# Optimization experiments

Hardware: AMD Instinct MI355X
Metric: run time of the kernel (lower is better)

## Reference

```python
import math
import jax, jax.numpy as jnp
import numpy as np

V, D, DEPTH, S, B = 32000, 1024, 4, 512, 2
N, K = 16, 4            # ssm state_dim, d_conv
R = math.ceil(D / 16)   # dt_rank ('auto') = 64
MLP = 4 * D


def _ln(x, s, b):
    m = jnp.mean(x, -1, keepdims=True)
    v = jnp.mean((x - m) ** 2, -1, keepdims=True)
    return (x - m) * jax.lax.rsqrt(v + 1e-5) * s + b


def _dwconv(x, w):
    # x: [B,S,D], w: [D,1,K]; causal depthwise conv (torch pads K-1 both sides then slices [:S])
    xt = jnp.transpose(x, (0, 2, 1))  # [B,D,S]
    y = jax.lax.conv_general_dilated(
        xt, w, window_strides=(1,), padding=[(K - 1, 0)],
        feature_group_count=D, dimension_numbers=('NCH', 'OIH', 'NCH'))
    return jnp.transpose(y, (0, 2, 1))


def _ssm(x, zw, pw, cw, dw, db, al, dpar, ow):
    z = x @ zw.T                     # [B,S,D]
    p = x @ pw.T                     # [B,S,R+2N]
    dt_un, Bp, Cp = p[..., :R], p[..., R:R + N], p[..., R + N:]
    dt = jax.nn.softplus(dt_un @ dw.T + db)          # [B,S,D]
    u = jax.nn.silu(_dwconv(x, cw))                  # [B,S,D]
    A = -jnp.exp(al)                                 # [D,N]
    At = jnp.exp(dt[..., None] * A)                  # [B,S,D,N]
    Bt = jnp.where(jnp.abs(A) < 1e-8, dt[..., None], (At - 1.0) / (A + 1e-10))
    inp = jnp.einsum('bsdn,bsn,bsd->bsdn', Bt, Bp, u)

    def step(h, xs):
        At_t, inp_t, C_t = xs
        h = At_t * h + inp_t
        return h, jnp.einsum('bn,bdn->bd', C_t, h)

    h0 = jnp.zeros((x.shape[0], D, N), x.dtype)
    _, ys = jax.lax.scan(step, h0, (jnp.moveaxis(At, 1, 0), jnp.moveaxis(inp, 1, 0), jnp.moveaxis(Cp, 1, 0)))
    y = jnp.moveaxis(ys, 0, 1)                       # [B,S,D]
    y = (y + u * dpar) * jax.nn.silu(z)
    return y @ ow.T


def _forward(input_ids, timesteps, tok_emb, time_w1, time_b1, time_w2, time_b2,
             norm1_s, norm1_b, xW, zW, pW, convW, dtW, dtb, A_log, Dp, outW,
             norm2_s, norm2_b, mlpW1, mlpb1, mlpW2, mlpb2, normo_s, normo_b, headW, headb):
    half = D // 2
    inv = jnp.exp(-(math.log(10000.0) / half) * jnp.arange(half, dtype=jnp.float32))
    args = timesteps.astype(jnp.float32)[:, None] * inv
    temb = jnp.concatenate([jnp.sin(args), jnp.cos(args)], axis=-1)        # [B,D]
    temb = jax.nn.silu(temb @ time_w1.T + time_b1) @ time_w2.T + time_b2
    x = tok_emb[input_ids] + temb[:, None, :]                              # [B,S,D]

    def block(x, prm):
        n1s, n1b, zw, pw, cw, dw, db, al, dpar, ow, n2s, n2b, w1, b1, w2, b2 = prm
        x = x + _ssm(_ln(x, n1s, n1b), zw, pw, cw, dw, db, al, dpar, ow)
        xn = _ln(x, n2s, n2b)
        x = x + (jax.nn.gelu(xn @ w1.T + b1, approximate=False) @ w2.T + b2)
        return x, None

    stacked = (norm1_s, norm1_b, zW, pW, convW, dtW, dtb, A_log, Dp, outW,
               norm2_s, norm2_b, mlpW1, mlpb1, mlpW2, mlpb2)
    x, _ = jax.lax.scan(block, x, stacked)
    x = _ln(x, normo_s, normo_b)
    return x @ headW.T + headb  # [B,S,V]


def setup_inputs():
    key = jax.random.key(0)
    ks = jax.random.split(key, 24)
    rn = lambda k, sh, sc=0.02: jax.random.normal(k, sh, jnp.float32) * sc
    dt_std = R ** (-0.5) * 0.1
    inp = {
        'input_ids': jax.random.randint(ks[0], (B, S), 0, V + 1),
        'timesteps': jax.random.randint(ks[1], (B,), 0, 100),
        'tok_emb': rn(ks[2], (V + 1, D)),
        'time_w1': rn(ks[3], (4 * D, D)), 'time_b1': jnp.zeros((4 * D,), jnp.float32),
        'time_w2': rn(ks[4], (D, 4 * D)), 'time_b2': jnp.zeros((D,), jnp.float32),
        'norm1_s': jnp.ones((DEPTH, D), jnp.float32), 'norm1_b': jnp.zeros((DEPTH, D), jnp.float32),
        'xW': rn(ks[5], (DEPTH, D, D)),   # in_proj_x (dead in forward, grad=0)
        'zW': rn(ks[6], (DEPTH, D, D)),
        'pW': rn(ks[7], (DEPTH, R + 2 * N, D)),
        'convW': rn(ks[8], (DEPTH, D, 1, K), 0.1),
        'dtW': jax.random.uniform(ks[9], (DEPTH, D, R), jnp.float32, -dt_std, dt_std),
        'dtb': jnp.full((DEPTH, D), math.log(math.expm1(0.001)), jnp.float32),
        'A_log': jnp.tile(jnp.log(jnp.arange(1, N + 1, dtype=jnp.float32))[None, None, :], (DEPTH, D, 1)),
        'Dp': jnp.ones((DEPTH, D), jnp.float32),
        'outW': rn(ks[10], (DEPTH, D, D)),
        'norm2_s': jnp.ones((DEPTH, D), jnp.float32), 'norm2_b': jnp.zeros((DEPTH, D), jnp.float32),
        'mlpW1': rn(ks[11], (DEPTH, MLP, D)), 'mlpb1': jnp.zeros((DEPTH, MLP), jnp.float32),
        'mlpW2': rn(ks[12], (DEPTH, D, MLP)), 'mlpb2': jnp.zeros((DEPTH, D), jnp.float32),
        'normo_s': jnp.ones((D,), jnp.float32), 'normo_b': jnp.zeros((D,), jnp.float32),
        'headW': rn(ks[13], (V, D)), 'headb': jnp.zeros((V,), jnp.float32),
    }
    return inp


def reference(input_ids, timesteps, tok_emb, time_w1, time_b1, time_w2, time_b2,
              norm1_s, norm1_b, xW, zW, pW, convW, dtW, dtb, A_log, Dp, outW,
              norm2_s, norm2_b, mlpW1, mlpb1, mlpW2, mlpb2, normo_s, normo_b, headW, headb):
    return _forward(input_ids, timesteps, tok_emb, time_w1, time_b1, time_w2, time_b2,
                    norm1_s, norm1_b, xW, zW, pW, convW, dtW, dtb, A_log, Dp, outW,
                    norm2_s, norm2_b, mlpW1, mlpb1, mlpW2, mlpb2, normo_s, normo_b, headW, headb)
```

## Files before the change

kernel.cpp:

```cpp
#include <hip/hip_runtime.h>
#include <math.h>


#define DEV __device__ __forceinline__
typedef unsigned int u32;
typedef unsigned short ushort;
typedef __bf16 bf16x8 __attribute__((ext_vector_type(8)));
typedef float f32x4 __attribute__((ext_vector_type(4)));
typedef ushort us8 __attribute__((ext_vector_type(8)));

DEV float silu_f(float x){ return x / (1.f + expf(-x)); }
DEV float gelu_f(float x){ return 0.5f * x * (1.f + erff(x * 0.70710678118654752f)); }
DEV float softplus_f(float x){ return (x > 20.f) ? x : log1pf(expf(x)); }
DEV ushort f2b(float f){
  u32 u = __builtin_bit_cast(u32, f);
  return (ushort)((u + 0x7fffu + ((u >> 16) & 1u)) >> 16);
}
DEV float b2f(ushort u){ return __builtin_bit_cast(float, (u32)u << 16); }

DEV void gl_lds16(const ushort* g, ushort* l){
  __builtin_amdgcn_global_load_lds(
      (const __attribute__((address_space(1))) u32*)g,
      (__attribute__((address_space(3))) u32*)l, 16, 0, 0);
}

DEV void cvt_layer_unit(u32 j, const float* zWl, const float* pWl, const float* oWl,
                        const float* m1Wl, const float* m2Wl, ushort* wl)
{
  const float* src; u32 sj, dj;
  if (j < 294912u){
    dj = j;
    u32 row = j >> 8;
    if (row < 1024u){ src = zWl; sj = j; }
    else {
      u32 pr = row - 1024u;
      if (pr >= 96u){ ushort4 z4 = {0,0,0,0}; ((ushort4*)wl)[dj] = z4; return; }
      src = pWl; sj = pr*256u + (j & 255u);
    }
  } else if (j < 557056u){ u32 k = j - 294912u;  dj = j; src = oWl;  sj = k; }
  else if (j < 1605632u){ u32 k = j - 557056u;  dj = j; src = m1Wl; sj = k; }
  else                  { u32 k = j - 1605632u; dj = j; src = m2Wl; sj = k; }
  float4 v = ((const float4*)src)[sj];
  ushort4 o4; o4.x=f2b(v.x); o4.y=f2b(v.y); o4.z=f2b(v.z); o4.w=f2b(v.w);
  ((ushort4*)wl)[dj] = o4;
}

__global__ __launch_bounds__(256) void k_cvtmega(
    const float* __restrict__ zW, const float* __restrict__ pW,
    const float* __restrict__ oW, const float* __restrict__ m1W,
    const float* __restrict__ m2W, const float* __restrict__ hW,
    ushort* __restrict__ wall, ushort* __restrict__ whb)
{
  u32 i = blockIdx.x*256u + threadIdx.x;
  if (i >= 18808832u) return;
  if (i >= 10616832u){
    u32 j = i - 10616832u;
    float4 v = ((const float4*)hW)[j];
    ushort4 o4; o4.x=f2b(v.x); o4.y=f2b(v.y); o4.z=f2b(v.z); o4.w=f2b(v.w);
    ((ushort4*)whb)[j] = o4;
    return;
  }
  u32 l = i / 2654208u;
  u32 j = i - l*2654208u;
  cvt_layer_unit(j, zW + (size_t)l*1048576u, pW + (size_t)l*98304u,
                 oW + (size_t)l*1048576u, m1W + (size_t)l*4194304u,
                 m2W + (size_t)l*4194304u, wall + (size_t)l*10616832u);
}

__global__ __launch_bounds__(256) void k_cvtall(
    const float* __restrict__ zWl, const float* __restrict__ pWl,
    const float* __restrict__ oWl, const float* __restrict__ m1Wl,
    const float* __restrict__ m2Wl, ushort* __restrict__ wl)
{
  u32 j = blockIdx.x*256u + threadIdx.x;
  if (j >= 2654208u) return;
  cvt_layer_unit(j, zWl, pWl, oWl, m1Wl, m2Wl, wl);
}

__global__ __launch_bounds__(256) void k_cvt(const float* __restrict__ in, ushort* __restrict__ out, int n4){
  int i = blockIdx.x*256 + threadIdx.x;
  if (i >= n4) return;
  float4 v = ((const float4*)in)[i];
  ushort4 o; o.x=f2b(v.x); o.y=f2b(v.y); o.z=f2b(v.z); o.w=f2b(v.w);
  ((ushort4*)out)[i] = o;
}

__global__ __launch_bounds__(256) void k_temb1m(const int* __restrict__ ts, const float* __restrict__ w1,
                                                const float* __restrict__ b1, float* __restrict__ t1){
  __shared__ float sXT[1024];
  int bid = blockIdx.x;
  int tid = threadIdx.x;
  int b = (bid*4) >> 12;
  float tv = (float)ts[b];
  #pragma unroll
  for (int k=0;k<4;k++){
    int j = tid + k*256;
    int i = j & 511;
    float arg = tv * expf(-(9.210340371976184f/512.f) * (float)i);
    sXT[j] = (j < 512) ? sinf(arg) : cosf(arg);
  }
  __syncthreads();
  int o = bid*4 + (tid >> 6);
  int lane = tid & 63;
  int j = o & 4095;
  const float4* xr = (const float4*)sXT;
  const float4* wr = (const float4*)(w1 + (size_t)j*1024);
  float acc = 0.f;
  #pragma unroll
  for (int i=0;i<4;i++){
    float4 x4 = xr[i*64 + lane], w4 = wr[i*64 + lane];
    acc += x4.x*w4.x + x4.y*w4.y + x4.z*w4.z + x4.w*w4.w;
  }
  #pragma unroll
  for (int off=32; off; off>>=1) acc += __shfl_down(acc, off);
  if (lane==0) t1[o] = silu_f(acc + b1[j]);
}

__global__ __launch_bounds__(256) void k_temb2(const float* __restrict__ t1, const float* __restrict__ w2,
                                               const float* __restrict__ b2, float* __restrict__ t2){
  int o = blockIdx.x*4 + (threadIdx.x >> 6);
  int lane = threadIdx.x & 63;
  int b = o >> 10, j = o & 1023;
  const float4* xr = (const float4*)(t1 + b*4096);
  const float4* wr = (const float4*)(w2 + (size_t)j*4096);
  float acc = 0.f;
  #pragma unroll
  for (int i=0;i<16;i++){
    float4 x4 = xr[i*64 + lane], w4 = wr[i*64 + lane];
    acc += x4.x*w4.x + x4.y*w4.y + x4.z*w4.z + x4.w*w4.w;
  }
  #pragma unroll
  for (int off=32; off; off>>=1) acc += __shfl_down(acc, off);
  if (lane==0) t2[o] = acc + b2[j];
}

DEV void ln_body(float4 v, const float* sc, const float* bi, int row, int t,
                 float* o, ushort* obf)
{
  float sum = v.x+v.y+v.z+v.w;
  float sq  = v.x*v.x+v.y*v.y+v.z*v.z+v.w*v.w;
  for (int o_=32;o_;o_>>=1){ sum += __shfl_down(sum,o_); sq += __shfl_down(sq,o_); }
  __shared__ float ps[8];
  int lane = t & 63, wid = t >> 6;
  if (lane==0){ ps[wid]=sum; ps[4+wid]=sq; }
  __syncthreads();
  float tot = ps[0]+ps[1]+ps[2]+ps[3];
  float tsq = ps[4]+ps[5]+ps[6]+ps[7];
  float m = tot * (1.f/1024.f);
  float var = tsq*(1.f/1024.f) - m*m;
  float r = rsqrtf(var + 1e-5f);
  float4 s4 = ((const float4*)sc)[t];
  float4 b4 = ((const float4*)bi)[t];
  float4 o4;
  o4.x = (v.x-m)*r*s4.x + b4.x;
  o4.y = (v.y-m)*r*s4.y + b4.y;
  o4.z = (v.z-m)*r*s4.z + b4.z;
  o4.w = (v.w-m)*r*s4.w + b4.w;
  ((float4*)(o + (size_t)row*1024))[t] = o4;
  ushort4 ob; ob.x=f2b(o4.x); ob.y=f2b(o4.y); ob.z=f2b(o4.z); ob.w=f2b(o4.w);
  ((ushort4*)(obf + (size_t)row*1024))[t] = ob;
}

__global__ __launch_bounds__(256) void k_ln(const float* __restrict__ x, const float* __restrict__ sc,
                                            const float* __restrict__ bi, float* __restrict__ o,
                                            ushort* __restrict__ obf){
  int row = blockIdx.x, t = threadIdx.x;
  float4 v = ((const float4*)(x + (size_t)row*1024))[t];
  ln_body(v, sc, bi, row, t, o, obf);
}

__global__ __launch_bounds__(256) void k_embln(const int* __restrict__ ids, const float* __restrict__ tok,
                                               const float* __restrict__ t2, const float* __restrict__ sc,
                                               const float* __restrict__ bi, float* __restrict__ xout,
                                               float* __restrict__ o, ushort* __restrict__ obf){
  int row = blockIdx.x, t = threadIdx.x;
  int id = ids[row];
  float4 v = ((const float4*)(tok + (size_t)id*1024))[t];
  float4 e = ((const float4*)(t2 + ((row >> 9) << 10)))[t];
  v.x += e.x; v.y += e.y; v.z += e.z; v.w += e.w;
  ((float4*)(xout + (size_t)row*1024))[t] = v;
  ln_body(v, sc, bi, row, t, o, obf);
}

__global__ __launch_bounds__(512) void k_scanf(
    const ushort* __restrict__ pb64, const float* __restrict__ dtW, const float* __restrict__ dtb,
    const float* __restrict__ xn, const float* __restrict__ p, const float* __restrict__ alog,
    const float* __restrict__ z, const float* __restrict__ Dp,
    const float* __restrict__ cw, ushort* __restrict__ y2b)
{
  const int bid = blockIdx.x;
  const int logical = (bid & 7)*256 + (bid >> 3);
  const int d = logical & 1023;
  const int b = logical >> 10;
  const int tid = threadIdx.x;
  const int c = tid >> 4, n = tid & 15;
  const float al = alog[d*16 + n];
  const float A = -expf(al);
  const float invA = 1.f/(A + 1e-10f);
  const bool tiny = fabsf(A) < 1e-8f;
  const float dscale = Dp[d];
  const float cw0 = cw[d*4], cw1 = cw[d*4+1], cw2 = cw[d*4+2], cw3 = cw[d*4+3];
  const size_t base = (size_t)b*512*1024 + d;
  const float* pp = p + (size_t)b*512*96;
  const int s0 = c*16;

  __shared__ float sXN[520];
  __shared__ float sDT[512], sZ[512];
  __shared__ float sA[512], sB[512], sH[512];
  __shared__ float sDTW[64];

  if (tid < 64) sDTW[tid] = dtW[d*64 + tid];
  {
    int s = tid - 3;
    sXN[tid] = (s >= 0) ? xn[base + (size_t)s*1024] : 0.f;
    if (tid < 3) sXN[512 + tid] = xn[base + (size_t)(509 + tid)*1024];
    sZ[tid] = z[base + (size_t)tid*1024];
  }
  __syncthreads();

  {
    const us8* pr = (const us8*)(pb64 + (size_t)(b*512 + tid)*64);
    float acc = 0.f;
    #pragma unroll
    for (int q=0;q<8;q++){
      us8 v = pr[q];
      #pragma unroll
      for (int e=0;e<8;e++)
        acc = fmaf(b2f(v[e]), sDTW[q*8+e], acc);
    }
    sDT[tid] = softplus_f(acc + dtb[d]);
  }
  __syncthreads();

  float At[16], inp[16];
  float h = 0.f, pa = 1.f;
  #pragma unroll
  for (int s8=0; s8<16; s8++){
    int s = s0 + s8;
    float uv = silu_f(sXN[s]*cw0 + sXN[s+1]*cw1 + sXN[s+2]*cw2 + sXN[s+3]*cw3);
    float dtv = sDT[s];
    float Bpv = pp[s*96 + 64 + n];
    float a  = expf(dtv*A);
    float bt = tiny ? dtv : (a-1.f)*invA;
    At[s8] = a;
    float ip = bt*Bpv*uv;
    inp[s8] = ip;
    h = a*h + ip;
    pa *= a;
  }
  sA[tid]=pa; sB[tid]=h;
  __syncthreads();
  if (tid < 16){
    float H = 0.f;
    #pragma unroll
    for (int c2=0;c2<32;c2++){
      sH[c2*16+tid] = H;
      H = sA[c2*16+tid]*H + sB[c2*16+tid];
    }
  }
  __syncthreads();

  h = sH[tid];
  #pragma unroll
  for (int s8=0; s8<16; s8++){
    int s = s0 + s8;
    h = At[s8]*h + inp[s8];
    float Cpv = pp[s*96 + 80 + n];
    float cc = Cpv*h;
    cc += __shfl_xor(cc,1);
    cc += __shfl_xor(cc,2);
    cc += __shfl_xor(cc,4);
    cc += __shfl_xor(cc,8);
    if (n==0){
      float uv = silu_f(sXN[s]*cw0 + sXN[s+1]*cw1 + sXN[s+2]*cw2 + sXN[s+3]*cw3);
      float zv = sZ[s];
      y2b[base + (size_t)s*1024] = f2b((cc + uv*dscale) * (zv/(1.f+expf(-zv))));
    }
  }
}

template<int TM, int TN, int EPI, bool OBF>
__global__ __launch_bounds__(256) void k_bgemm(
    const ushort* __restrict__ A,
    const ushort* __restrict__ W,
    const float* __restrict__ bias,
    const float* __restrict__ resid,
    void* __restrict__ Cout,
    int ldc, int nmax, int K,
    float* __restrict__ pout, ushort* __restrict__ pbout)
{
  constexpr int WN = 2;
  constexpr int WM = 2;
  constexpr int MR = TM/(WM*16);
  constexpr int NR = TN/(WN*16);

  __shared__ ushort As[TM*64] __attribute__((aligned(16)));
  __shared__ ushort Bs[TN*64] __attribute__((aligned(16)));
  const int t = threadIdx.x;
  const int w = t >> 6, lane = t & 63;
  const int wn = w % WN, wm = w / WN;
  const int m0 = blockIdx.y * TM;
  const int n0 = blockIdx.x * TN;

  f32x4 acc[MR][NR];
  #pragma unroll
  for (int i=0;i<MR;i++)
    #pragma unroll
    for (int j=0;j<NR;j++) acc[i][j] = (f32x4){0.f,0.f,0.f,0.f};

  const int srow = (lane >> 3);
  const int scol = (((lane & 7) ^ srow)) * 8;

  for (int k0 = 0; k0 < K; k0 += 64){
    __syncthreads();
    #pragma unroll
    for (int i=0;i<TM/32;i++){
      int chunk = i*4 + w;
      int row = chunk*8 + srow;
      gl_lds16(A + (size_t)(m0 + row)*K + k0 + scol, &As[chunk*512]);
    }
    #pragma unroll
    for (int i=0;i<TN/32;i++){
      int chunk = i*4 + w;
      int row = chunk*8 + srow;
      gl_lds16(W + (size_t)(n0 + row)*K + k0 + scol, &Bs[chunk*512]);
    }
    __syncthreads();
    const int fr = lane & 15;
    const int hi = lane >> 4;
    #pragma unroll
    for (int kk=0; kk<2; ++kk){
      bf16x8 a[MR], b[NR];
      const int cofs = (((kk<<2) | hi) ^ (fr & 7)) * 8;
      #pragma unroll
      for (int am=0; am<MR; am++)
        a[am] = *(const bf16x8*)&As[(wm*(MR*16) + am*16 + fr)*64 + cofs];
      #pragma unroll
      for (int bn=0; bn<NR; bn++)
        b[bn] = *(const bf16x8*)&Bs[(wn*(NR*16) + bn*16 + fr)*64 + cofs];
      #pragma unroll
      for (int am=0; am<MR; am++)
        #pragma unroll
        for (int bn=0; bn<NR; bn++)
          acc[am][bn] = __builtin_amdgcn_mfma_f32_16x16x32_bf16(a[am], b[bn], acc[am][bn], 0, 0, 0);
    }
  }

  #pragma unroll
  for (int am=0; am<MR; am++){
    #pragma unroll
    for (int bn=0; bn<NR; bn++){
      int r0 = m0 + wm*(MR*16) + am*16 + ((lane>>4)<<2);
      int cc = n0 + wn*(NR*16) + bn*16 + (lane&15);
      if (cc >= nmax) continue;
      float bv = 0.f;
      if constexpr (EPI==1 || EPI==2 || EPI==5) bv = bias[cc];
      #pragma unroll
      for (int r=0; r<4; r++){
        float v = acc[am][bn][r];
        if constexpr (EPI==1 || EPI==2 || EPI==5) v += bv;
        if constexpr (EPI==2) v = gelu_f(v);
        if constexpr (EPI==4 || EPI==5) v += resid[(size_t)(r0+r)*ldc + cc];
        if constexpr (EPI==6){
          if (cc < 1024) ((float*)Cout)[(size_t)(r0+r)*ldc + cc] = v;
          else {
            int pc = cc - 1024;
            if (pc < 96) pout[(size_t)(r0+r)*96 + pc] = v;
            if (pc < 64) pbout[(size_t)(r0+r)*64 + pc] = f2b(v);
          }
        } else if constexpr (OBF){
          ((ushort*)Cout)[(size_t)(r0+r)*ldc + cc] = f2b(v);
        } else {
          ((float*)Cout)[(size_t)(r0+r)*ldc + cc] = v;
        }
      }
    }
  }
}

__global__ __launch_bounds__(512) void k_bgemmH(
    const ushort* __restrict__ A,
    const ushort* __restrict__ W,
    const float* __restrict__ bias,
    float* __restrict__ Cout,
    int ldc, int K)
{
  __shared__ ushort As[256*64] __attribute__((aligned(16)));
  __shared__ ushort Bs[128*64] __attribute__((aligned(16)));
  const int t = threadIdx.x;
  const int w = t >> 6, lane = t & 63;
  const int wn = w & 1, wm = w >> 1;
  const int bid = blockIdx.x;
  const int logical = (bid & 7)*125 + (bid >> 3);
  const int m0 = (logical & 3) * 256;
  const int n0 = (logical >> 2) * 128;

  f32x4 acc[4][4];
  #pragma unroll
  for (int i=0;i<4;i++)
    #pragma unroll
    for (int j=0;j<4;j++) acc[i][j] = (f32x4){0.f,0.f,0.f,0.f};

  const int srow = (lane >> 3);
  const int scol = (((lane & 7) ^ srow)) * 8;

  for (int k0 = 0; k0 < K; k0 += 64){
    __syncthreads();
    #pragma unroll
    for (int i=0;i<4;i++){
      int chunk = i*8 + w;
      int row = chunk*8 + srow;
      gl_lds16(A + (size_t)(m0 + row)*K + k0 + scol, &As[chunk*512]);
    }
    #pragma unroll
    for (int i=0;i<2;i++){
      int chunk = i*8 + w;
      int row = chunk*8 + srow;
      gl_lds16(W + (size_t)(n0 + row)*K + k0 + scol, &Bs[chunk*512]);
    }
    __syncthreads();
    const int fr = lane & 15;
    const int hi = lane >> 4;
    #pragma unroll
    for (int kk=0; kk<2; ++kk){
      bf16x8 a[4], b[4];
      const int cofs = (((kk<<2) | hi) ^ (fr & 7)) * 8;
      #pragma unroll
      for (int am=0; am<4; am++)
        a[am] = *(const bf16x8*)&As[(wm*64 + am*16 + fr)*64 + cofs];
      #pragma unroll
      for (int bn=0; bn<4; bn++)
        b[bn] = *(const bf16x8*)&Bs[(wn*64 + bn*16 + fr)*64 + cofs];
      #pragma unroll
      for (int am=0; am<4; am++)
        #pragma unroll
        for (int bn=0; bn<4; bn++)
          acc[am][bn] = __builtin_amdgcn_mfma_f32_16x16x32_bf16(a[am], b[bn], acc[am][bn], 0, 0, 0);
    }
  }

  #pragma unroll
  for (int am=0; am<4; am++){
    #pragma unroll
    for (int bn=0; bn<4; bn++){
      int r0 = m0 + wm*64 + am*16 + ((lane>>4)<<2);
      int cc = n0 + wn*64 + bn*16 + (lane&15);
      float bv = bias[cc];
      #pragma unroll
      for (int r=0; r<4; r++)
        Cout[(size_t)(r0+r)*ldc + cc] = acc[am][bn][r] + bv;
    }
  }
}

extern "C" void kernel_launch(void* const* d_in, const int* in_sizes, int n_in,
                              void* d_out, int out_size, void* d_ws, size_t ws_size,
                              hipStream_t stream)
{
  const int*   ids    = (const int*)d_in[0];
  const int*   tsteps = (const int*)d_in[1];
  const float* tok    = (const float*)d_in[2];
  const float* tw1    = (const float*)d_in[3];
  const float* tb1    = (const float*)d_in[4];
  const float* tw2    = (const float*)d_in[5];
  const float* tb2    = (const float*)d_in[6];
  const float* n1s    = (const float*)d_in[7];
  const float* n1b    = (const float*)d_in[8];
  const float* zW     = (const float*)d_in[10];
  const float* pW     = (const float*)d_in[11];
  const float* cW     = (const float*)d_in[12];
  const float* dtW    = (const float*)d_in[13];
  const float* dtb    = (const float*)d_in[14];
  const float* alog   = (const float*)d_in[15];
  const float* Dp     = (const float*)d_in[16];
  const float* oW     = (const float*)d_in[17];
  const float* n2s    = (const float*)d_in[18];
  const float* n2b    = (const float*)d_in[19];
  const float* m1W    = (const float*)d_in[20];
  const float* m1b    = (const float*)d_in[21];
  const float* m2W    = (const float*)d_in[22];
  const float* m2b    = (const float*)d_in[23];
  const float* nos    = (const float*)d_in[24];
  const float* nob    = (const float*)d_in[25];
  const float* hW     = (const float*)d_in[26];
  const float* hb     = (const float*)d_in[27];

  float* ws = (float*)d_ws;
  float*  x    = ws;
  float*  xn   = ws + 1048576;
  float*  z    = ws + 2097152;
  float*  p    = ws + 3145728;
  ushort* pb64 = (ushort*)(ws + 3244032);
  float*  t1   = ws + 3276800;
  float*  t2   = ws + 3284992;
  ushort* xnb  = (ushort*)(ws + 3670016);
  ushort* y2b  = (ushort*)(ws + 4194304);
  ushort* h1b  = (ushort*)(ws + 5242880);

  const size_t WBASE = 7340032;
  const size_t WL_US = 10616832;
  const bool big = ws_size >= 179830784ull;
  ushort* wall = (ushort*)(ws + WBASE);
  ushort* whb  = big ? (ushort*)(ws + WBASE + 4*(WL_US/2))
                     : (ushort*)(ws + WBASE);

  dim3 blk(256);
  if (big)
    k_cvtmega<<<dim3(73472), blk, 0, stream>>>(zW, pW, oW, m1W, m2W, hW, wall, whb);
  k_temb1m<<<dim3(2048), blk, 0, stream>>>(tsteps, tw1, tb1, t1);
  k_temb2<<<dim3(512),  blk, 0, stream>>>(t1, tw2, tb2, t2);

  for (int l=0; l<4; l++){
    ushort* wl = wall + (big ? (size_t)l*WL_US : 0);
    ushort* wzp = wl;
    ushort* wo  = wl + 1179648;
    ushort* wm1 = wl + 2228224;
    ushort* wm2 = wl + 6422528;
    if (!big)
      k_cvtall<<<dim3(10368), blk, 0, stream>>>(
          zW + (size_t)l*1048576, pW + (size_t)l*98304, oW + (size_t)l*1048576,
          m1W + (size_t)l*4194304, m2W + (size_t)l*4194304, wl);
    if (l == 0)
      k_embln<<<dim3(1024), blk, 0, stream>>>(ids, tok, t2, n1s, n1b, x, xn, xnb);
    else
      k_ln<<<dim3(1024), blk, 0, stream>>>(x, n1s + l*1024, n1b + l*1024, xn, xnb);
    k_bgemm<64,64,6,false><<<dim3(18,16), blk, 0, stream>>>(xnb, wzp, nullptr, nullptr, z,
                                                            1024, 1152, 1024, p, pb64);
    k_scanf<<<dim3(2048), dim3(512), 0, stream>>>(pb64, dtW + (size_t)l*65536, dtb + l*1024,
                                                  xn, p, alog + l*16384, z, Dp + l*1024,
                                                  cW + l*4096, y2b);
    k_bgemm<64,64,4,false><<<dim3(16,16), blk, 0, stream>>>(y2b, wo, nullptr, x, x,
                                                            1024, 1024, 1024, nullptr, nullptr);
    k_ln<<<dim3(1024), blk, 0, stream>>>(x, n2s + l*1024, n2b + l*1024, xn, xnb);
    k_bgemm<128,128,2,true><<<dim3(32,8), blk, 0, stream>>>(xnb, wm1, m1b + l*4096, nullptr, h1b,
                                                            4096, 4096, 1024, nullptr, nullptr);
    k_bgemm<64,64,5,false><<<dim3(16,16), blk, 0, stream>>>(h1b, wm2, m2b + l*1024, x, x,
                                                            1024, 1024, 4096, nullptr, nullptr);
  }
  k_ln<<<dim3(1024), blk, 0, stream>>>(x, nos, nob, xn, xnb);

  if (big){
    k_bgemmH<<<dim3(1000), dim3(512), 0, stream>>>(xnb, whb, hb, (float*)d_out, 32000, 1024);
  } else {
    for (int h=0; h<2; h++){
      k_cvt<<<dim3(16000), blk, 0, stream>>>(hW + (size_t)h*16384000, whb, 4096000);
      k_bgemm<128,128,1,false><<<dim3(125,8), blk, 0, stream>>>(xnb, whb, hb + h*16000, nullptr,
                                                                (float*)d_out + h*16000,
                                                                32000, 16000, 1024, nullptr, nullptr);
    }
  }
}
```

Before: 1.042 ms.

## Fuse head weight fp32-to-bf16 conversion into head GEMM and retile MLP1 GEMM

The head GEMM now reads fp32 head weights directly, converts them to bf16 in registers, and stores them into swizzled LDS. The next k-tile is prefetched into registers and synchronisation is done with manual waitcnt and barriers. This removes the separate conversion pass over the large head weight matrix from the mega-convert kernel, so its write and reread of a bf16 copy disappear. The MLP up-projection GEMM also switches from 128x128 to 64x64 tiles with a larger grid, trading per-block reuse for more blocks. The fp32 B loads double the global traffic for the head weights inside the GEMM.

```diff
diff --git a/kernel.cpp b/kernel.cpp
--- a/kernel.cpp
+++ b/kernel.cpp
@@ -22,6 +22,13 @@
   __builtin_amdgcn_global_load_lds(
       (const __attribute__((address_space(1))) u32*)g,
       (__attribute__((address_space(3))) u32*)l, 16, 0, 0);
+}
+
+DEV us8 cvt2(float4 a, float4 b){
+  us8 v;
+  v[0]=f2b(a.x); v[1]=f2b(a.y); v[2]=f2b(a.z); v[3]=f2b(a.w);
+  v[4]=f2b(b.x); v[5]=f2b(b.y); v[6]=f2b(b.z); v[7]=f2b(b.w);
+  return v;
 }
 
 DEV void cvt_layer_unit(u32 j, const float* zWl, const float* pWl, const float* oWl,
@@ -48,18 +55,10 @@
 __global__ __launch_bounds__(256) void k_cvtmega(
     const float* __restrict__ zW, const float* __restrict__ pW,
     const float* __restrict__ oW, const float* __restrict__ m1W,
-    const float* __restrict__ m2W, const float* __restrict__ hW,
-    ushort* __restrict__ wall, ushort* __restrict__ whb)
+    const float* __restrict__ m2W, ushort* __restrict__ wall)
 {
   u32 i = blockIdx.x*256u + threadIdx.x;
-  if (i >= 18808832u) return;
-  if (i >= 10616832u){
-    u32 j = i - 10616832u;
-    float4 v = ((const float4*)hW)[j];
-    ushort4 o4; o4.x=f2b(v.x); o4.y=f2b(v.y); o4.z=f2b(v.z); o4.w=f2b(v.w);
-    ((ushort4*)whb)[j] = o4;
-    return;
-  }
+  if (i >= 10616832u) return;
   u32 l = i / 2654208u;
   u32 j = i - l*2654208u;
   cvt_layer_unit(j, zW + (size_t)l*1048576u, pW + (size_t)l*98304u,
@@ -378,9 +377,9 @@
   }
 }
 
-__global__ __launch_bounds__(512) void k_bgemmH(
+__global__ __launch_bounds__(512) void k_bgemmHF(
     const ushort* __restrict__ A,
-    const ushort* __restrict__ W,
+    const float*  __restrict__ W,
     const float* __restrict__ bias,
     float* __restrict__ Cout,
     int ldc, int K)
@@ -402,7 +401,17 @@
     for (int j=0;j<4;j++) acc[i][j] = (f32x4){0.f,0.f,0.f,0.f};
 
   const int srow = (lane >> 3);
-  const int scol = (((lane & 7) ^ srow)) * 8;
+  const int scolA = (((lane & 7) ^ srow)) * 8;
+
+  const int brow = t >> 2;
+  const int bq   = t & 3;
+  const float* wp = W + (size_t)(n0 + brow)*K + bq*16;
+  const int slot0 = ((bq*2)   ^ (brow & 7)) * 8;
+  const int slot1 = ((bq*2+1) ^ (brow & 7)) * 8;
+
+  float4 fb[4];
+  #pragma unroll
+  for (int j=0;j<4;j++) fb[j] = *(const float4*)(wp + j*4);
 
   for (int k0 = 0; k0 < K; k0 += 64){
     __syncthreads();
@@ -410,15 +419,20 @@
     for (int i=0;i<4;i++){
       int chunk = i*8 + w;
       int row = chunk*8 + srow;
-      gl_lds16(A + (size_t)(m0 + row)*K + k0 + scol, &As[chunk*512]);
-    }
-    #pragma unroll
-    for (int i=0;i<2;i++){
-      int chunk = i*8 + w;
-      int row = chunk*8 + srow;
-      gl_lds16(W + (size_t)(n0 + row)*K + k0 + scol, &Bs[chunk*512]);
-    }
-    __syncthreads();
+      gl_lds16(A + (size_t)(m0 + row)*K + k0 + scolA, &As[chunk*512]);
+    }
+    *(us8*)&Bs[brow*64 + slot0] = cvt2(fb[0], fb[1]);
+    *(us8*)&Bs[brow*64 + slot1] = cvt2(fb[2], fb[3]);
+    if (k0 + 64 < K){
+      #pragma unroll
+      for (int j=0;j<4;j++) fb[j] = *(const float4*)(wp + k0 + 64 + j*4);
+      asm volatile("s_waitcnt vmcnt(4) lgkmcnt(0)" ::: "memory");
+    } else {
+      asm volatile("s_waitcnt vmcnt(0) lgkmcnt(0)" ::: "memory");
+    }
+    __builtin_amdgcn_sched_barrier(0);
+    __builtin_amdgcn_s_barrier();
+    __builtin_amdgcn_sched_barrier(0);
     const int fr = lane & 15;
     const int hi = lane >> 4;
     #pragma unroll
@@ -501,12 +515,11 @@
   const size_t WL_US = 10616832;
   const bool big = ws_size >= 179830784ull;
   ushort* wall = (ushort*)(ws + WBASE);
-  ushort* whb  = big ? (ushort*)(ws + WBASE + 4*(WL_US/2))
-                     : (ushort*)(ws + WBASE);
+  ushort* whb  = (ushort*)(ws + WBASE + (big ? 4*(WL_US/2) : 0));
 
   dim3 blk(256);
   if (big)
-    k_cvtmega<<<dim3(73472), blk, 0, stream>>>(zW, pW, oW, m1W, m2W, hW, wall, whb);
+    k_cvtmega<<<dim3(41472), blk, 0, stream>>>(zW, pW, oW, m1W, m2W, wall);
   k_temb1m<<<dim3(2048), blk, 0, stream>>>(tsteps, tw1, tb1, t1);
   k_temb2<<<dim3(512),  blk, 0, stream>>>(t1, tw2, tb2, t2);
 
@@ -532,15 +545,15 @@
     k_bgemm<64,64,4,false><<<dim3(16,16), blk, 0, stream>>>(y2b, wo, nullptr, x, x,
                                                             1024, 1024, 1024, nullptr, nullptr);
     k_ln<<<dim3(1024), blk, 0, stream>>>(x, n2s + l*1024, n2b + l*1024, xn, xnb);
-    k_bgemm<128,128,2,true><<<dim3(32,8), blk, 0, stream>>>(xnb, wm1, m1b + l*4096, nullptr, h1b,
-                                                            4096, 4096, 1024, nullptr, nullptr);
+    k_bgemm<64,64,2,true><<<dim3(64,16), blk, 0, stream>>>(xnb, wm1, m1b + l*4096, nullptr, h1b,
+                                                           4096, 4096, 1024, nullptr, nullptr);
     k_bgemm<64,64,5,false><<<dim3(16,16), blk, 0, stream>>>(h1b, wm2, m2b + l*1024, x, x,
                                                             1024, 1024, 4096, nullptr, nullptr);
   }
   k_ln<<<dim3(1024), blk, 0, stream>>>(x, nos, nob, xn, xnb);
 
   if (big){
-    k_bgemmH<<<dim3(1000), dim3(512), 0, stream>>>(xnb, whb, hb, (float*)d_out, 32000, 1024);
+    k_bgemmHF<<<dim3(1000), dim3(512), 0, stream>>>(xnb, hW, hb, (float*)d_out, 32000, 1024);
   } else {
     for (int h=0; h<2; h++){
       k_cvt<<<dim3(16000), blk, 0, stream>>>(hW + (size_t)h*16384000, whb, 4096000);
```

Measured after the change: 890.9 us. 14.5% less time.
